# Performance work log

Measured on AMD Instinct MI355X. Metric: run time of the kernel, lower is better.

The kernel has to match this reference:

```python
import jax, jax.numpy as jnp
import numpy as np

L = 2          # MPblock_layers
H = 64         # hidden_channels
B, N, E = 1, 50000, 800000


def setup_inputs() -> dict:
    key = jax.random.key(0)
    ks = jax.random.split(key, 12)
    s = 0.05
    return {
        "x": jax.random.normal(ks[0], (B, N, H), jnp.float32),
        "edge_attr": jax.random.normal(ks[1], (B, E, H), jnp.float32),
        "edge_index": jax.random.randint(ks[2], (2, E), 0, N, jnp.int64 if jax.config.jax_enable_x64 else jnp.int32),
        # per-layer stacked MLP params: edge MLP (3H->H->H), node MLP (2H->H->H)
        "edge_w1": jax.random.normal(ks[3], (L, 3 * H, H), jnp.float32) * s,
        "edge_b1": jnp.zeros((L, H), jnp.float32),
        "edge_w2": jax.random.normal(ks[4], (L, H, H), jnp.float32) * s,
        "edge_b2": jnp.zeros((L, H), jnp.float32),
        "node_w1": jax.random.normal(ks[5], (L, 2 * H, H), jnp.float32) * s,
        "node_b1": jnp.zeros((L, H), jnp.float32),
        "node_w2": jax.random.normal(ks[6], (L, H, H), jnp.float32) * s,
        "node_b2": jnp.zeros((L, H), jnp.float32),
    }


def reference(x, edge_attr, edge_index,
              edge_w1, edge_b1, edge_w2, edge_b2,
              node_w1, node_b1, node_w2, node_b2):
    src = edge_index[0]
    dest = edge_index[1]
    n_nodes = x.shape[1]
    for l in range(L):
        # EdgeModel: cat([edge_attr, x[src], x[dest]]) -> MLP
        cat_e = jnp.concatenate([edge_attr, x[:, src], x[:, dest]], axis=2)  # [B,E,3H]
        h = jax.nn.silu(jnp.einsum('bef,fh->beh', cat_e, edge_w1[l]) + edge_b1[l])
        edge_attr = jnp.einsum('beh,hk->bek', h, edge_w2[l]) + edge_b2[l]      # [B,E,H]
        # NodeModel: scatter_add over dest, cat with x, MLP
        agg = jnp.zeros((x.shape[0], n_nodes, edge_attr.shape[2]), x.dtype).at[:, dest].add(edge_attr)
        cat_n = jnp.concatenate([x, agg], axis=2)                              # [B,N,2H]
        h = jax.nn.silu(jnp.einsum('bnf,fh->bnh', cat_n, node_w1[l]) + node_b1[l])
        x = jnp.einsum('bnh,hk->bnk', h, node_w2[l]) + node_b2[l]              # [B,N,H]
    return (x, edge_attr)
```

## Files before the change

kernel.cpp:

```cpp
#include <hip/hip_runtime.h>

typedef __attribute__((ext_vector_type(8))) _Float16 f16x8;
typedef __attribute__((ext_vector_type(4))) _Float16 f16x4;
typedef __attribute__((ext_vector_type(4))) float f32x4;

#define PWS 72

__device__ __forceinline__ float silu_f(float v) {
    return v * (1.0f / (1.0f + __expf(-v)));
}

__device__ __forceinline__ int xcd_swz(int bid, int nwg) {
    if (nwg < 16) return bid;
    int q = nwg >> 3, r = nwg & 7;
    int x = bid & 7, i = bid >> 3;
    int basex = (x < r) ? x * (q + 1) : r * (q + 1) + (x - r) * q;
    return basex + i;
}

struct WDesc { const float* W; _Float16* out; int K; };
struct WPack { WDesc d[8]; };

__global__ __launch_bounds__(256) void conv_weights(WPack p) {
    WDesc wd = p.d[blockIdx.y];
    int total = wd.K * 64;
    int i = blockIdx.x * 256 + threadIdx.x;
    if (i >= total) return;
    int j  = i & 7;
    int l  = (i >> 3) & 63;
    int tn = i >> 9;
    int t  = tn >> 2, nf = tn & 3;
    int k  = t * 32 + (l >> 4) * 8 + j;
    int c  = nf * 16 + (l & 15);
    wd.out[i] = (_Float16)wd.W[k * 64 + c];
}

__global__ __launch_bounds__(256) void hist_kernel(const int* __restrict__ dst,
                                                   int* __restrict__ counts, int E) {
    int e = blockIdx.x * 256 + threadIdx.x;
    if (e < E) atomicAdd(&counts[dst[e]], 1);
}

__global__ __launch_bounds__(1024) void scan_kernel(int* __restrict__ counts,
                                                    int* __restrict__ row_ptr,
                                                    int N, int E) {
    __shared__ int part[1024];
    int t = threadIdx.x;
    int per = (N + 1023) >> 10;
    int s = t * per, en = min(s + per, N);
    int sum = 0;
    for (int i = s; i < en; ++i) sum += counts[i];
    part[t] = sum;
    __syncthreads();
    for (int off = 1; off < 1024; off <<= 1) {
        int v = (t >= off) ? part[t - off] : 0;
        __syncthreads();
        part[t] += v;
        __syncthreads();
    }
    int run = (t == 0) ? 0 : part[t - 1];
    for (int i = s; i < en; ++i) {
        int c = counts[i];
        row_ptr[i] = run;
        counts[i] = run;
        run += c;
    }
    if (t == 1023) row_ptr[N] = E;
}

__global__ __launch_bounds__(256) void scatter_kernel(
    const int* __restrict__ src, const int* __restrict__ dst,
    int* __restrict__ cursor, int4* __restrict__ pk, int E) {
    int e = blockIdx.x * 256 + threadIdx.x;
    if (e < E) {
        int d = dst[e];
        int pos = atomicAdd(&cursor[d], 1);
        pk[pos] = make_int4(e, src[e], d, 0);
    }
}

template <bool IN16, bool FINAL>
__global__ __launch_bounds__(256, 8) void gnn_edge_sorted(
    const float* __restrict__ x,
    const float* __restrict__ ea0,
    _Float16* __restrict__ ea_mid,
    float* __restrict__ ea_out,
    const int4* __restrict__ pk,
    const _Float16* __restrict__ w1f,
    const float* __restrict__ b1,
    const _Float16* __restrict__ w2f,
    const float* __restrict__ b2,
    int E, int nwg)
{
    __shared__ __align__(16) _Float16 sA[64][PWS];

    const int t    = threadIdx.x;
    const int lane = t & 63;
    const int w    = t >> 6;
    const int col  = lane & 15;
    const int g    = lane >> 4;
    const int ko   = g * 8;
    const int bid  = xcd_swz(blockIdx.x, nwg);
    const long base = (long)bid * 64;

    long p0 = base + w * 16 + col;
    if (p0 >= E) p0 = E - 1;
    int ei0 = 0;
    if constexpr (FINAL) ei0 = pk[p0].x;

    f16x4  ea16v[4];
    float4 ea4[4];
    float4 sx4[4], dx4[4];
#pragma unroll
    for (int it = 0; it < 4; ++it) {
        long p = base + w * 16 + it * 4 + g;
        if (p >= E) p = E - 1;
        int4 rec = pk[p];
        if constexpr (IN16) {
            ea16v[it] = *(const f16x4*)(ea_mid + p * 64 + col * 4);
        } else {
            ea4[it] = *(const float4*)(ea0 + (long)rec.x * 64 + col * 4);
        }
        sx4[it] = *(const float4*)(x + (long)rec.y * 64 + col * 4);
        dx4[it] = *(const float4*)(x + (long)rec.z * 64 + col * 4);
    }

    f32x4 acc[4];
#pragma unroll
    for (int nf = 0; nf < 4; ++nf) {
        float bv = b1[nf * 16 + col];
        acc[nf] = (f32x4){bv, bv, bv, bv};
    }

    const int arow = w * 16 + col;

#define MFMA_L1(s3)                                                             \
    _Pragma("unroll")                                                           \
    for (int tt = 0; tt < 2; ++tt) {                                            \
        int k0 = tt * 32 + ko;                                                  \
        f16x8 af = *(const f16x8*)&sA[arow][k0];                                \
        int tg = (s3) * 2 + tt;                                                 \
        _Pragma("unroll")                                                       \
        for (int nf = 0; nf < 4; ++nf) {                                        \
            f16x8 bf = *(const f16x8*)(w1f + (size_t)((tg*4+nf)*64+lane)*8);    \
            acc[nf] = __builtin_amdgcn_mfma_f32_16x16x32_f16(af, bf, acc[nf], 0, 0, 0); \
        }                                                                       \
    }

#pragma unroll
    for (int it = 0; it < 4; ++it) {
        int rg = w * 16 + it * 4 + g;
        f16x4 hv;
        if constexpr (IN16) {
            hv = ea16v[it];
        } else {
            hv[0] = (_Float16)ea4[it].x; hv[1] = (_Float16)ea4[it].y;
            hv[2] = (_Float16)ea4[it].z; hv[3] = (_Float16)ea4[it].w;
        }
        *(f16x4*)&sA[rg][col * 4] = hv;
    }
    MFMA_L1(0)

#pragma unroll
    for (int it = 0; it < 4; ++it) {
        int rg = w * 16 + it * 4 + g;
        f16x4 hv;
        hv[0] = (_Float16)sx4[it].x; hv[1] = (_Float16)sx4[it].y;
        hv[2] = (_Float16)sx4[it].z; hv[3] = (_Float16)sx4[it].w;
        *(f16x4*)&sA[rg][col * 4] = hv;
    }
    MFMA_L1(1)

#pragma unroll
    for (int it = 0; it < 4; ++it) {
        int rg = w * 16 + it * 4 + g;
        f16x4 hv;
        hv[0] = (_Float16)dx4[it].x; hv[1] = (_Float16)dx4[it].y;
        hv[2] = (_Float16)dx4[it].z; hv[3] = (_Float16)dx4[it].w;
        *(f16x4*)&sA[rg][col * 4] = hv;
    }
    MFMA_L1(2)
#undef MFMA_L1

#pragma unroll
    for (int nf = 0; nf < 4; ++nf)
#pragma unroll
        for (int rg = 0; rg < 4; ++rg) {
            int row = w * 16 + g * 4 + rg;
            sA[row][nf * 16 + col] = (_Float16)silu_f(acc[nf][rg]);
        }

    f32x4 out[4];
#pragma unroll
    for (int nf = 0; nf < 4; ++nf) {
        float bv = b2[nf * 16 + col];
        out[nf] = (f32x4){bv, bv, bv, bv};
    }
#pragma unroll
    for (int tt = 0; tt < 2; ++tt) {
        int k0 = tt * 32 + ko;
        f16x8 af = *(const f16x8*)&sA[arow][k0];
#pragma unroll
        for (int nf = 0; nf < 4; ++nf) {
            f16x8 bf = *(const f16x8*)(w2f + (size_t)((tt * 4 + nf) * 64 + lane) * 8);
            out[nf] = __builtin_amdgcn_mfma_f32_16x16x32_f16(af, bf, out[nf], 0, 0, 0);
        }
    }

    const int rbase = w * 16 + g * 4;
#pragma unroll
    for (int rg = 0; rg < 4; ++rg) {
        long p = base + rbase + rg;
        if (p < E) {
#pragma unroll
            for (int nf = 0; nf < 4; ++nf)
                ea_mid[p * 64 + nf * 16 + col] = (_Float16)out[nf][rg];
            if constexpr (FINAL) {
                int eid = __shfl(ei0, g * 4 + rg);
                float* op = ea_out + (long)eid * 64;
#pragma unroll
                for (int nf = 0; nf < 4; ++nf)
                    op[nf * 16 + col] = out[nf][rg];
            }
        }
    }
}

__global__ __launch_bounds__(256, 4) void gnn_node_fused(
    const float* __restrict__ x_in,
    const _Float16* __restrict__ eaH,
    const int* __restrict__ row_ptr,
    float* __restrict__ x_out,
    const _Float16* __restrict__ w1f,
    const float* __restrict__ b1,
    const _Float16* __restrict__ w2f,
    const float* __restrict__ b2, int N, int nwg)
{
    __shared__ __align__(16) _Float16 sA[64][PWS];

    const int t    = threadIdx.x;
    const int lane = t & 63;
    const int w    = t >> 6;
    const int col  = lane & 15;
    const int g    = lane >> 4;
    const int ko   = g * 8;
    const int bid  = xcd_swz(blockIdx.x, nwg);
    const long base = (long)bid * 64;

    long nr = base + w * 16 + col;
    if (nr >= N) nr = N - 1;
    const float* px = x_in + nr * 64 + ko;

    float4 v0 = *(const float4*)(px);
    float4 v1 = *(const float4*)(px + 4);
    float4 v2 = *(const float4*)(px + 32);
    float4 v3 = *(const float4*)(px + 36);

    int pe0 = row_ptr[nr], pe1 = row_ptr[nr + 1];
    float s0[8], s1[8];
#pragma unroll
    for (int j = 0; j < 8; ++j) { s0[j] = 0.f; s1[j] = 0.f; }
    for (int p = pe0; p < pe1; ++p) {
        f16x8 a = *(const f16x8*)(eaH + (long)p * 64 + ko);
        f16x8 b = *(const f16x8*)(eaH + (long)p * 64 + 32 + ko);
#pragma unroll
        for (int j = 0; j < 8; ++j) { s0[j] += (float)a[j]; s1[j] += (float)b[j]; }
    }

    f32x4 acc[4];
#pragma unroll
    for (int nf = 0; nf < 4; ++nf) {
        float bv = b1[nf * 16 + col];
        acc[nf] = (f32x4){bv, bv, bv, bv};
    }

#define QTRV(m, A, B)                                                           \
    {                                                                           \
        f16x8 af;                                                               \
        af[0] = (_Float16)A.x; af[1] = (_Float16)A.y;                           \
        af[2] = (_Float16)A.z; af[3] = (_Float16)A.w;                           \
        af[4] = (_Float16)B.x; af[5] = (_Float16)B.y;                           \
        af[6] = (_Float16)B.z; af[7] = (_Float16)B.w;                           \
        _Pragma("unroll")                                                       \
        for (int nf = 0; nf < 4; ++nf) {                                        \
            f16x8 bf = *(const f16x8*)(w1f + (size_t)(((m)*4+nf)*64+lane)*8);   \
            acc[nf] = __builtin_amdgcn_mfma_f32_16x16x32_f16(af, bf, acc[nf], 0, 0, 0); \
        }                                                                       \
    }
#define QTRS(m, S)                                                              \
    {                                                                           \
        f16x8 af;                                                               \
        _Pragma("unroll")                                                       \
        for (int j = 0; j < 8; ++j) af[j] = (_Float16)S[j];                     \
        _Pragma("unroll")                                                       \
        for (int nf = 0; nf < 4; ++nf) {                                        \
            f16x8 bf = *(const f16x8*)(w1f + (size_t)(((m)*4+nf)*64+lane)*8);   \
            acc[nf] = __builtin_amdgcn_mfma_f32_16x16x32_f16(af, bf, acc[nf], 0, 0, 0); \
        }                                                                       \
    }
    QTRV(0, v0, v1)  QTRV(1, v2, v3)
    QTRS(2, s0)      QTRS(3, s1)
#undef QTRV
#undef QTRS

#pragma unroll
    for (int nf = 0; nf < 4; ++nf)
#pragma unroll
        for (int rg = 0; rg < 4; ++rg) {
            int row = w * 16 + g * 4 + rg;
            sA[row][nf * 16 + col] = (_Float16)silu_f(acc[nf][rg]);
        }

    f32x4 out[4];
#pragma unroll
    for (int nf = 0; nf < 4; ++nf) {
        float bv = b2[nf * 16 + col];
        out[nf] = (f32x4){bv, bv, bv, bv};
    }
    const int arow = w * 16 + col;
#pragma unroll
    for (int tt = 0; tt < 2; ++tt) {
        int k0 = tt * 32 + ko;
        f16x8 af = *(const f16x8*)&sA[arow][k0];
#pragma unroll
        for (int nf = 0; nf < 4; ++nf) {
            f16x8 bf = *(const f16x8*)(w2f + (size_t)((tt * 4 + nf) * 64 + lane) * 8);
            out[nf] = __builtin_amdgcn_mfma_f32_16x16x32_f16(af, bf, out[nf], 0, 0, 0);
        }
    }

    const int rbase = w * 16 + g * 4;
#pragma unroll
    for (int rg = 0; rg < 4; ++rg) {
        long row = base + rbase + rg;
        if (row < N) {
            float* op = x_out + row * 64;
#pragma unroll
            for (int nf = 0; nf < 4; ++nf)
                op[nf * 16 + col] = out[nf][rg];
        }
    }
}

__global__ __launch_bounds__(256, 8) void gnn_edge_mfma(
    const float* __restrict__ x,
    const float* __restrict__ ea_in,
    float* __restrict__ ea_out,
    const int* __restrict__ src_idx,
    const int* __restrict__ dst_idx,
    const _Float16* __restrict__ w1f,
    const float* __restrict__ b1,
    const _Float16* __restrict__ w2f,
    const float* __restrict__ b2,
    float* __restrict__ agg,
    int E)
{
    __shared__ __align__(16) _Float16 sA[64][PWS];

    const int t    = threadIdx.x;
    const int lane = t & 63;
    const int w    = t >> 6;
    const int col  = lane & 15;
    const int g    = lane >> 4;
    const int ko   = g * 8;
    const long base = (long)blockIdx.x * 64;

    long er0 = base + w * 16 + col;
    if (er0 >= E) er0 = E - 1;
    const int di = dst_idx[er0];

    float4 ea4[4], sx4[4], dx4[4];
#pragma unroll
    for (int it = 0; it < 4; ++it) {
        long er = base + w * 16 + it * 4 + g;
        if (er >= E) er = E - 1;
        ea4[it] = *(const float4*)(ea_in + er * 64 + col * 4);
        sx4[it] = *(const float4*)(x + (long)src_idx[er] * 64 + col * 4);
        dx4[it] = *(const float4*)(x + (long)dst_idx[er] * 64 + col * 4);
    }

    f32x4 acc[4];
#pragma unroll
    for (int nf = 0; nf < 4; ++nf) {
        float bv = b1[nf * 16 + col];
        acc[nf] = (f32x4){bv, bv, bv, bv};
    }
    const int arow = w * 16 + col;

#define MFMA_L1(s3)                                                             \
    _Pragma("unroll")                                                           \
    for (int tt = 0; tt < 2; ++tt) {                                            \
        int k0 = tt * 32 + ko;                                                  \
        f16x8 af = *(const f16x8*)&sA[arow][k0];                                \
        int tg = (s3) * 2 + tt;                                                 \
        _Pragma("unroll")                                                       \
        for (int nf = 0; nf < 4; ++nf) {                                        \
            f16x8 bf = *(const f16x8*)(w1f + (size_t)((tg*4+nf)*64+lane)*8);    \
            acc[nf] = __builtin_amdgcn_mfma_f32_16x16x32_f16(af, bf, acc[nf], 0, 0, 0); \
        }                                                                       \
    }

#pragma unroll
    for (int it = 0; it < 4; ++it) {
        int rg = w * 16 + it * 4 + g;
        f16x4 hv;
        hv[0] = (_Float16)ea4[it].x; hv[1] = (_Float16)ea4[it].y;
        hv[2] = (_Float16)ea4[it].z; hv[3] = (_Float16)ea4[it].w;
        *(f16x4*)&sA[rg][col * 4] = hv;
    }
    MFMA_L1(0)
#pragma unroll
    for (int it = 0; it < 4; ++it) {
        int rg = w * 16 + it * 4 + g;
        f16x4 hv;
        hv[0] = (_Float16)sx4[it].x; hv[1] = (_Float16)sx4[it].y;
        hv[2] = (_Float16)sx4[it].z; hv[3] = (_Float16)sx4[it].w;
        *(f16x4*)&sA[rg][col * 4] = hv;
    }
    MFMA_L1(1)
#pragma unroll
    for (int it = 0; it < 4; ++it) {
        int rg = w * 16 + it * 4 + g;
        f16x4 hv;
        hv[0] = (_Float16)dx4[it].x; hv[1] = (_Float16)dx4[it].y;
        hv[2] = (_Float16)dx4[it].z; hv[3] = (_Float16)dx4[it].w;
        *(f16x4*)&sA[rg][col * 4] = hv;
    }
    MFMA_L1(2)
#undef MFMA_L1

#pragma unroll
    for (int nf = 0; nf < 4; ++nf)
#pragma unroll
        for (int rg = 0; rg < 4; ++rg) {
            int row = w * 16 + g * 4 + rg;
            sA[row][nf * 16 + col] = (_Float16)silu_f(acc[nf][rg]);
        }

    f32x4 out[4];
#pragma unroll
    for (int nf = 0; nf < 4; ++nf) {
        float bv = b2[nf * 16 + col];
        out[nf] = (f32x4){bv, bv, bv, bv};
    }
#pragma unroll
    for (int tt = 0; tt < 2; ++tt) {
        int k0 = tt * 32 + ko;
        f16x8 af = *(const f16x8*)&sA[arow][k0];
#pragma unroll
        for (int nf = 0; nf < 4; ++nf) {
            f16x8 bf = *(const f16x8*)(w2f + (size_t)((tt * 4 + nf) * 64 + lane) * 8);
            out[nf] = __builtin_amdgcn_mfma_f32_16x16x32_f16(af, bf, out[nf], 0, 0, 0);
        }
    }

    const int rbase = w * 16 + g * 4;
#pragma unroll
    for (int rg = 0; rg < 4; ++rg) {
        long row = base + rbase + rg;
        if (row < E) {
            int drow = __shfl(di, g * 4 + rg);
            float* ap = agg + (long)drow * 64;
#pragma unroll
            for (int nf = 0; nf < 4; ++nf) {
                ea_out[row * 64 + nf * 16 + col] = out[nf][rg];
                atomicAdd(&ap[nf * 16 + col], out[nf][rg]);
            }
        }
    }
}

__global__ __launch_bounds__(256, 8) void gnn_node_mfma(
    const float* __restrict__ x_in,
    const float* __restrict__ aggp,
    float* __restrict__ x_out,
    const _Float16* __restrict__ w1f,
    const float* __restrict__ b1,
    const _Float16* __restrict__ w2f,
    const float* __restrict__ b2, int N)
{
    __shared__ __align__(16) _Float16 sA[64][PWS];

    const int t    = threadIdx.x;
    const int lane = t & 63;
    const int w    = t >> 6;
    const int col  = lane & 15;
    const int g    = lane >> 4;
    const int ko   = g * 8;
    const long base = (long)blockIdx.x * 64;

    long nr = base + w * 16 + col;
    if (nr >= N) nr = N - 1;
    const float* px = x_in + nr * 64 + ko;
    const float* pa = aggp + nr * 64 + ko;

    float4 v0 = *(const float4*)(px);
    float4 v1 = *(const float4*)(px + 4);
    float4 v2 = *(const float4*)(px + 32);
    float4 v3 = *(const float4*)(px + 36);
    float4 v4 = *(const float4*)(pa);
    float4 v5 = *(const float4*)(pa + 4);
    float4 v6 = *(const float4*)(pa + 32);
    float4 v7 = *(const float4*)(pa + 36);

    f32x4 acc[4];
#pragma unroll
    for (int nf = 0; nf < 4; ++nf) {
        float bv = b1[nf * 16 + col];
        acc[nf] = (f32x4){bv, bv, bv, bv};
    }

#define QTR(m, A, B)                                                            \
    {                                                                           \
        f16x8 af;                                                               \
        af[0] = (_Float16)A.x; af[1] = (_Float16)A.y;                           \
        af[2] = (_Float16)A.z; af[3] = (_Float16)A.w;                           \
        af[4] = (_Float16)B.x; af[5] = (_Float16)B.y;                           \
        af[6] = (_Float16)B.z; af[7] = (_Float16)B.w;                           \
        _Pragma("unroll")                                                       \
        for (int nf = 0; nf < 4; ++nf) {                                        \
            f16x8 bf = *(const f16x8*)(w1f + (size_t)(((m)*4+nf)*64+lane)*8);   \
            acc[nf] = __builtin_amdgcn_mfma_f32_16x16x32_f16(af, bf, acc[nf], 0, 0, 0); \
        }                                                                       \
    }
    QTR(0, v0, v1)  QTR(1, v2, v3)
    QTR(2, v4, v5)  QTR(3, v6, v7)
#undef QTR

#pragma unroll
    for (int nf = 0; nf < 4; ++nf)
#pragma unroll
        for (int rg = 0; rg < 4; ++rg) {
            int row = w * 16 + g * 4 + rg;
            sA[row][nf * 16 + col] = (_Float16)silu_f(acc[nf][rg]);
        }

    f32x4 out[4];
#pragma unroll
    for (int nf = 0; nf < 4; ++nf) {
        float bv = b2[nf * 16 + col];
        out[nf] = (f32x4){bv, bv, bv, bv};
    }
    const int arow = w * 16 + col;
#pragma unroll
    for (int tt = 0; tt < 2; ++tt) {
        int k0 = tt * 32 + ko;
        f16x8 af = *(const f16x8*)&sA[arow][k0];
#pragma unroll
        for (int nf = 0; nf < 4; ++nf) {
            f16x8 bf = *(const f16x8*)(w2f + (size_t)((tt * 4 + nf) * 64 + lane) * 8);
            out[nf] = __builtin_amdgcn_mfma_f32_16x16x32_f16(af, bf, out[nf], 0, 0, 0);
        }
    }

    const int rbase = w * 16 + g * 4;
#pragma unroll
    for (int rg = 0; rg < 4; ++rg) {
        long row = base + rbase + rg;
        if (row < N) {
            float* op = x_out + row * 64;
#pragma unroll
            for (int nf = 0; nf < 4; ++nf)
                op[nf * 16 + col] = out[nf][rg];
        }
    }
}

extern "C" void kernel_launch(void* const* d_in, const int* in_sizes, int n_in,
                              void* d_out, int out_size, void* d_ws, size_t ws_size,
                              hipStream_t stream) {
    const int H = 64;
    const int N = in_sizes[0] / H;
    const int E = in_sizes[1] / H;

    const float* x0  = (const float*)d_in[0];
    const float* ea0 = (const float*)d_in[1];
    const int*   ei  = (const int*)d_in[2];
    const float* ew1 = (const float*)d_in[3];
    const float* eb1 = (const float*)d_in[4];
    const float* ew2 = (const float*)d_in[5];
    const float* eb2 = (const float*)d_in[6];
    const float* nw1 = (const float*)d_in[7];
    const float* nb1 = (const float*)d_in[8];
    const float* nw2 = (const float*)d_in[9];
    const float* nb2 = (const float*)d_in[10];

    float* outX = (float*)d_out;
    float* outE = outX + (size_t)N * H;

    const size_t aggBytes = (size_t)N * H * sizeof(float);
    const size_t wElems   = 2 * ((size_t)(192 + 64 + 128 + 64) * 64);
    const size_t eaHBytes = (size_t)E * H * sizeof(_Float16);

    float* agg      = (float*)d_ws;
    _Float16* wbase = (_Float16*)((char*)d_ws + aggBytes);
    char* eaH_raw   = (char*)(wbase + wElems);
    eaH_raw = (char*)(((uintptr_t)eaH_raw + 15) & ~(uintptr_t)15);
    _Float16* eaH   = (_Float16*)eaH_raw;
    int* counts     = (int*)(((uintptr_t)((char*)eaH + eaHBytes) + 15) & ~(uintptr_t)15);
    int* row_ptr    = counts + N;
    int4* pk        = (int4*)(((uintptr_t)(row_ptr + N + 1) + 15) & ~(uintptr_t)15);

    const bool sortedOK = ((char*)(pk + E)) <= ((char*)d_ws + ws_size);

    const int* srcI = ei;
    const int* dstI = ei + E;

    WPack pack;
    size_t off = 0;
    _Float16* EW1[2]; _Float16* EW2[2]; _Float16* NW1[2]; _Float16* NW2[2];
    for (int l = 0; l < 2; ++l) {
        EW1[l] = wbase + off; off += 192 * 64;
        EW2[l] = wbase + off; off += 64 * 64;
        NW1[l] = wbase + off; off += 128 * 64;
        NW2[l] = wbase + off; off += 64 * 64;
        pack.d[l * 4 + 0] = {ew1 + (size_t)l * 192 * 64, EW1[l], 192};
        pack.d[l * 4 + 1] = {ew2 + (size_t)l * 64 * 64,  EW2[l], 64};
        pack.d[l * 4 + 2] = {nw1 + (size_t)l * 128 * 64, NW1[l], 128};
        pack.d[l * 4 + 3] = {nw2 + (size_t)l * 64 * 64,  NW2[l], 64};
    }
    conv_weights<<<dim3(48, 8), 256, 0, stream>>>(pack);

    const int egrid = (E + 63) / 64;
    const int ngrid = (N + 63) / 64;

    if (sortedOK) {
        (void)hipMemsetAsync(counts, 0, (size_t)N * sizeof(int), stream);
        hist_kernel<<<(E + 255) / 256, 256, 0, stream>>>(dstI, counts, E);
        scan_kernel<<<1, 1024, 0, stream>>>(counts, row_ptr, N, E);
        scatter_kernel<<<(E + 255) / 256, 256, 0, stream>>>(
            srcI, dstI, counts, pk, E);

        gnn_edge_sorted<false, false><<<egrid, 256, 0, stream>>>(
            x0, ea0, eaH, nullptr, pk,
            EW1[0], eb1, EW2[0], eb2, E, egrid);
        gnn_node_fused<<<ngrid, 256, 0, stream>>>(
            x0, eaH, row_ptr, outX, NW1[0], nb1, NW2[0], nb2, N, ngrid);

        gnn_edge_sorted<true, true><<<egrid, 256, 0, stream>>>(
            outX, nullptr, eaH, outE, pk,
            EW1[1], eb1 + H, EW2[1], eb2 + H, E, egrid);
        gnn_node_fused<<<ngrid, 256, 0, stream>>>(
            outX, eaH, row_ptr, outX, NW1[1], nb1 + H, NW2[1], nb2 + H, N, ngrid);
    } else {
        for (int l = 0; l < 2; ++l) {
            const float* xin  = (l == 0) ? x0  : outX;
            const float* eain = (l == 0) ? ea0 : outE;
            (void)hipMemsetAsync(agg, 0, aggBytes, stream);
            gnn_edge_mfma<<<egrid, 256, 0, stream>>>(
                xin, eain, outE, srcI, dstI,
                EW1[l], eb1 + l * H, EW2[l], eb2 + l * H, agg, E);
            gnn_node_mfma<<<ngrid, 256, 0, stream>>>(
                xin, agg, outX,
                NW1[l], nb1 + l * H, NW2[l], nb2 + l * H, N);
        }
    }
}
```

Baseline: 558.5 us.

## Parallelize CSR scan, read layer-1 edges in original order, unroll aggregation

Measured after the change: 472.2 us. 15.4% less time.

```diff
diff --git a/kernel.cpp b/kernel.cpp
--- a/kernel.cpp
+++ b/kernel.cpp
@@ -41,55 +41,78 @@
     if (e < E) atomicAdd(&counts[dst[e]], 1);
 }
 
-__global__ __launch_bounds__(1024) void scan_kernel(int* __restrict__ counts,
-                                                    int* __restrict__ row_ptr,
-                                                    int N, int E) {
-    __shared__ int part[1024];
+__global__ __launch_bounds__(256) void scan_part(const int* __restrict__ counts,
+                                                 int* __restrict__ partial, int N) {
+    __shared__ int sm[256];
     int t = threadIdx.x;
-    int per = (N + 1023) >> 10;
-    int s = t * per, en = min(s + per, N);
-    int sum = 0;
-    for (int i = s; i < en; ++i) sum += counts[i];
-    part[t] = sum;
+    int i = blockIdx.x * 256 + t;
+    sm[t] = (i < N) ? counts[i] : 0;
     __syncthreads();
-    for (int off = 1; off < 1024; off <<= 1) {
-        int v = (t >= off) ? part[t - off] : 0;
+    for (int off = 128; off > 0; off >>= 1) {
+        if (t < off) sm[t] += sm[t + off];
         __syncthreads();
-        part[t] += v;
+    }
+    if (t == 0) partial[blockIdx.x] = sm[0];
+}
+
+__global__ __launch_bounds__(256) void scan_mid(int* __restrict__ partial, int nP) {
+    __shared__ int sm[256];
+    int t = threadIdx.x;
+    int v = (t < nP) ? partial[t] : 0;
+    sm[t] = v;
+    __syncthreads();
+    for (int off = 1; off < 256; off <<= 1) {
+        int add = (t >= off) ? sm[t - off] : 0;
         __syncthreads();
-    }
-    int run = (t == 0) ? 0 : part[t - 1];
-    for (int i = s; i < en; ++i) {
-        int c = counts[i];
-        row_ptr[i] = run;
-        counts[i] = run;
-        run += c;
-    }
-    if (t == 1023) row_ptr[N] = E;
+        sm[t] += add;
+        __syncthreads();
+    }
+    if (t < nP) partial[t] = sm[t] - v;
+}
+
+__global__ __launch_bounds__(256) void scan_fin(int* __restrict__ counts,
+                                                const int* __restrict__ partial,
+                                                int* __restrict__ row_ptr,
+                                                int N, int E) {
+    __shared__ int sm[256];
+    int t = threadIdx.x;
+    int i = blockIdx.x * 256 + t;
+    int v = (i < N) ? counts[i] : 0;
+    sm[t] = v;
+    __syncthreads();
+    for (int off = 1; off < 256; off <<= 1) {
+        int add = (t >= off) ? sm[t - off] : 0;
+        __syncthreads();
+        sm[t] += add;
+        __syncthreads();
+    }
+    int excl = sm[t] - v + partial[blockIdx.x];
+    if (i < N) { row_ptr[i] = excl; counts[i] = excl; }
+    if (blockIdx.x == 0 && t == 0) row_ptr[N] = E;
 }
 
 __global__ __launch_bounds__(256) void scatter_kernel(
     const int* __restrict__ src, const int* __restrict__ dst,
-    int* __restrict__ cursor, int4* __restrict__ pk, int E) {
+    int* __restrict__ cursor, int4* __restrict__ pk,
+    int* __restrict__ posA, int E) {
     int e = blockIdx.x * 256 + threadIdx.x;
     if (e < E) {
         int d = dst[e];
         int pos = atomicAdd(&cursor[d], 1);
         pk[pos] = make_int4(e, src[e], d, 0);
-    }
-}
-
-template <bool IN16, bool FINAL>
-__global__ __launch_bounds__(256, 8) void gnn_edge_sorted(
+        posA[e] = pos;
+    }
+}
+
+__global__ __launch_bounds__(256, 8) void gnn_edge_l1(
     const float* __restrict__ x,
-    const float* __restrict__ ea0,
+    const float* __restrict__ ea_in,
     _Float16* __restrict__ ea_mid,
-    float* __restrict__ ea_out,
-    const int4* __restrict__ pk,
-    const _Float16* __restrict__ w1f,
-    const float* __restrict__ b1,
-    const _Float16* __restrict__ w2f,
-    const float* __restrict__ b2,
+    const int* __restrict__ src_idx,
+    const int* __restrict__ dst_idx,
+    const int* __restrict__ posA,
+    const _Float16* __restrict__ w1f, const float* __restrict__ b1,
+    const _Float16* __restrict__ w2f, const float* __restrict__ b2,
     int E, int nwg)
 {
     __shared__ __align__(16) _Float16 sA[64][PWS];
@@ -103,26 +126,18 @@
     const int bid  = xcd_swz(blockIdx.x, nwg);
     const long base = (long)bid * 64;
 
-    long p0 = base + w * 16 + col;
-    if (p0 >= E) p0 = E - 1;
-    int ei0 = 0;
-    if constexpr (FINAL) ei0 = pk[p0].x;
-
-    f16x4  ea16v[4];
-    float4 ea4[4];
-    float4 sx4[4], dx4[4];
-#pragma unroll
-    for (int it = 0; it < 4; ++it) {
-        long p = base + w * 16 + it * 4 + g;
-        if (p >= E) p = E - 1;
-        int4 rec = pk[p];
-        if constexpr (IN16) {
-            ea16v[it] = *(const f16x4*)(ea_mid + p * 64 + col * 4);
-        } else {
-            ea4[it] = *(const float4*)(ea0 + (long)rec.x * 64 + col * 4);
-        }
-        sx4[it] = *(const float4*)(x + (long)rec.y * 64 + col * 4);
-        dx4[it] = *(const float4*)(x + (long)rec.z * 64 + col * 4);
+    long er0 = base + w * 16 + col;
+    if (er0 >= E) er0 = E - 1;
+    const int p0 = posA[er0];
+
+    float4 ea4[4], sx4[4], dx4[4];
+#pragma unroll
+    for (int it = 0; it < 4; ++it) {
+        long er = base + w * 16 + it * 4 + g;
+        if (er >= E) er = E - 1;
+        ea4[it] = *(const float4*)(ea_in + er * 64 + col * 4);
+        sx4[it] = *(const float4*)(x + (long)src_idx[er] * 64 + col * 4);
+        dx4[it] = *(const float4*)(x + (long)dst_idx[er] * 64 + col * 4);
     }
 
     f32x4 acc[4];
@@ -131,7 +146,6 @@
         float bv = b1[nf * 16 + col];
         acc[nf] = (f32x4){bv, bv, bv, bv};
     }
-
     const int arow = w * 16 + col;
 
 #define MFMA_L1(s3)                                                             \
@@ -151,16 +165,11 @@
     for (int it = 0; it < 4; ++it) {
         int rg = w * 16 + it * 4 + g;
         f16x4 hv;
-        if constexpr (IN16) {
-            hv = ea16v[it];
-        } else {
-            hv[0] = (_Float16)ea4[it].x; hv[1] = (_Float16)ea4[it].y;
-            hv[2] = (_Float16)ea4[it].z; hv[3] = (_Float16)ea4[it].w;
-        }
+        hv[0] = (_Float16)ea4[it].x; hv[1] = (_Float16)ea4[it].y;
+        hv[2] = (_Float16)ea4[it].z; hv[3] = (_Float16)ea4[it].w;
         *(f16x4*)&sA[rg][col * 4] = hv;
     }
     MFMA_L1(0)
-
 #pragma unroll
     for (int it = 0; it < 4; ++it) {
         int rg = w * 16 + it * 4 + g;
@@ -170,7 +179,6 @@
         *(f16x4*)&sA[rg][col * 4] = hv;
     }
     MFMA_L1(1)
-
 #pragma unroll
     for (int it = 0; it < 4; ++it) {
         int rg = w * 16 + it * 4 + g;
@@ -210,31 +218,24 @@
     const int rbase = w * 16 + g * 4;
 #pragma unroll
     for (int rg = 0; rg < 4; ++rg) {
-        long p = base + rbase + rg;
-        if (p < E) {
+        long row = base + rbase + rg;
+        if (row < E) {
+            int pp = __shfl(p0, g * 4 + rg);
 #pragma unroll
             for (int nf = 0; nf < 4; ++nf)
-                ea_mid[p * 64 + nf * 16 + col] = (_Float16)out[nf][rg];
-            if constexpr (FINAL) {
-                int eid = __shfl(ei0, g * 4 + rg);
-                float* op = ea_out + (long)eid * 64;
-#pragma unroll
-                for (int nf = 0; nf < 4; ++nf)
-                    op[nf * 16 + col] = out[nf][rg];
-            }
-        }
-    }
-}
-
-__global__ __launch_bounds__(256, 4) void gnn_node_fused(
-    const float* __restrict__ x_in,
-    const _Float16* __restrict__ eaH,
-    const int* __restrict__ row_ptr,
-    float* __restrict__ x_out,
-    const _Float16* __restrict__ w1f,
-    const float* __restrict__ b1,
-    const _Float16* __restrict__ w2f,
-    const float* __restrict__ b2, int N, int nwg)
+                ea_mid[(long)pp * 64 + nf * 16 + col] = (_Float16)out[nf][rg];
+        }
+    }
+}
+
+__global__ __launch_bounds__(256, 8) void gnn_edge_l2(
+    const float* __restrict__ x,
+    _Float16* __restrict__ ea_mid,
+    float* __restrict__ ea_out,
+    const int4* __restrict__ pk,
+    const _Float16* __restrict__ w1f, const float* __restrict__ b1,
+    const _Float16* __restrict__ w2f, const float* __restrict__ b2,
+    int E, int nwg)
 {
     __shared__ __align__(16) _Float16 sA[64][PWS];
 
@@ -247,6 +248,131 @@
     const int bid  = xcd_swz(blockIdx.x, nwg);
     const long base = (long)bid * 64;
 
+    long p0 = base + w * 16 + col;
+    if (p0 >= E) p0 = E - 1;
+    const int ei0 = pk[p0].x;
+
+    f16x4  ea16v[4];
+    float4 sx4[4], dx4[4];
+#pragma unroll
+    for (int it = 0; it < 4; ++it) {
+        long p = base + w * 16 + it * 4 + g;
+        if (p >= E) p = E - 1;
+        int4 rec = pk[p];
+        ea16v[it] = *(const f16x4*)(ea_mid + p * 64 + col * 4);
+        sx4[it] = *(const float4*)(x + (long)rec.y * 64 + col * 4);
+        dx4[it] = *(const float4*)(x + (long)rec.z * 64 + col * 4);
+    }
+
+    f32x4 acc[4];
+#pragma unroll
+    for (int nf = 0; nf < 4; ++nf) {
+        float bv = b1[nf * 16 + col];
+        acc[nf] = (f32x4){bv, bv, bv, bv};
+    }
+    const int arow = w * 16 + col;
+
+#define MFMA_L1(s3)                                                             \
+    _Pragma("unroll")                                                           \
+    for (int tt = 0; tt < 2; ++tt) {                                            \
+        int k0 = tt * 32 + ko;                                                  \
+        f16x8 af = *(const f16x8*)&sA[arow][k0];                                \
+        int tg = (s3) * 2 + tt;                                                 \
+        _Pragma("unroll")                                                       \
+        for (int nf = 0; nf < 4; ++nf) {                                        \
+            f16x8 bf = *(const f16x8*)(w1f + (size_t)((tg*4+nf)*64+lane)*8);    \
+            acc[nf] = __builtin_amdgcn_mfma_f32_16x16x32_f16(af, bf, acc[nf], 0, 0, 0); \
+        }                                                                       \
+    }
+
+#pragma unroll
+    for (int it = 0; it < 4; ++it) {
+        int rg = w * 16 + it * 4 + g;
+        *(f16x4*)&sA[rg][col * 4] = ea16v[it];
+    }
+    MFMA_L1(0)
+#pragma unroll
+    for (int it = 0; it < 4; ++it) {
+        int rg = w * 16 + it * 4 + g;
+        f16x4 hv;
+        hv[0] = (_Float16)sx4[it].x; hv[1] = (_Float16)sx4[it].y;
+        hv[2] = (_Float16)sx4[it].z; hv[3] = (_Float16)sx4[it].w;
+        *(f16x4*)&sA[rg][col * 4] = hv;
+    }
+    MFMA_L1(1)
+#pragma unroll
+    for (int it = 0; it < 4; ++it) {
+        int rg = w * 16 + it * 4 + g;
+        f16x4 hv;
+        hv[0] = (_Float16)dx4[it].x; hv[1] = (_Float16)dx4[it].y;
+        hv[2] = (_Float16)dx4[it].z; hv[3] = (_Float16)dx4[it].w;
+        *(f16x4*)&sA[rg][col * 4] = hv;
+    }
+    MFMA_L1(2)
+#undef MFMA_L1
+
+#pragma unroll
+    for (int nf = 0; nf < 4; ++nf)
+#pragma unroll
+        for (int rg = 0; rg < 4; ++rg) {
+            int row = w * 16 + g * 4 + rg;
+            sA[row][nf * 16 + col] = (_Float16)silu_f(acc[nf][rg]);
+        }
+
+    f32x4 out[4];
+#pragma unroll
+    for (int nf = 0; nf < 4; ++nf) {
+        float bv = b2[nf * 16 + col];
+        out[nf] = (f32x4){bv, bv, bv, bv};
+    }
+#pragma unroll
+    for (int tt = 0; tt < 2; ++tt) {
+        int k0 = tt * 32 + ko;
+        f16x8 af = *(const f16x8*)&sA[arow][k0];
+#pragma unroll
+        for (int nf = 0; nf < 4; ++nf) {
+            f16x8 bf = *(const f16x8*)(w2f + (size_t)((tt * 4 + nf) * 64 + lane) * 8);
+            out[nf] = __builtin_amdgcn_mfma_f32_16x16x32_f16(af, bf, out[nf], 0, 0, 0);
+        }
+    }
+
+    const int rbase = w * 16 + g * 4;
+#pragma unroll
+    for (int rg = 0; rg < 4; ++rg) {
+        long p = base + rbase + rg;
+        if (p < E) {
+#pragma unroll
+            for (int nf = 0; nf < 4; ++nf)
+                ea_mid[p * 64 + nf * 16 + col] = (_Float16)out[nf][rg];
+            int eid = __shfl(ei0, g * 4 + rg);
+            float* op = ea_out + (long)eid * 64;
+#pragma unroll
+            for (int nf = 0; nf < 4; ++nf)
+                op[nf * 16 + col] = out[nf][rg];
+        }
+    }
+}
+
+__global__ __launch_bounds__(256, 4) void gnn_node_fused(
+    const float* __restrict__ x_in,
+    const _Float16* __restrict__ eaH,
+    const int* __restrict__ row_ptr,
+    float* __restrict__ x_out,
+    const _Float16* __restrict__ w1f, const float* __restrict__ b1,
+    const _Float16* __restrict__ w2f, const float* __restrict__ b2,
+    int N, int nwg)
+{
+    __shared__ __align__(16) _Float16 sA[64][PWS];
+
+    const int t    = threadIdx.x;
+    const int lane = t & 63;
+    const int w    = t >> 6;
+    const int col  = lane & 15;
+    const int g    = lane >> 4;
+    const int ko   = g * 8;
+    const int bid  = xcd_swz(blockIdx.x, nwg);
+    const long base = (long)bid * 64;
+
     long nr = base + w * 16 + col;
     if (nr >= N) nr = N - 1;
     const float* px = x_in + nr * 64 + ko;
@@ -260,11 +386,23 @@
     float s0[8], s1[8];
 #pragma unroll
     for (int j = 0; j < 8; ++j) { s0[j] = 0.f; s1[j] = 0.f; }
-    for (int p = pe0; p < pe1; ++p) {
-        f16x8 a = *(const f16x8*)(eaH + (long)p * 64 + ko);
-        f16x8 b = *(const f16x8*)(eaH + (long)p * 64 + 32 + ko);
-#pragma unroll
-        for (int j = 0; j < 8; ++j) { s0[j] += (float)a[j]; s1[j] += (float)b[j]; }
+    int p = pe0;
+    for (; p + 2 <= pe1; p += 2) {
+        f16x8 a0 = *(const f16x8*)(eaH + (long)p * 64 + ko);
+        f16x8 b0 = *(const f16x8*)(eaH + (long)p * 64 + 32 + ko);
+        f16x8 a1 = *(const f16x8*)(eaH + (long)(p + 1) * 64 + ko);
+        f16x8 b1v = *(const f16x8*)(eaH + (long)(p + 1) * 64 + 32 + ko);
+#pragma unroll
+        for (int j = 0; j < 8; ++j) {
+            s0[j] += (float)a0[j] + (float)a1[j];
+            s1[j] += (float)b0[j] + (float)b1v[j];
+        }
+    }
+    if (p < pe1) {
+        f16x8 a0 = *(const f16x8*)(eaH + (long)p * 64 + ko);
+        f16x8 b0 = *(const f16x8*)(eaH + (long)p * 64 + 32 + ko);
+#pragma unroll
+        for (int j = 0; j < 8; ++j) { s0[j] += (float)a0[j]; s1[j] += (float)b0[j]; }
     }
 
     f32x4 acc[4];
@@ -348,12 +486,9 @@
     float* __restrict__ ea_out,
     const int* __restrict__ src_idx,
     const int* __restrict__ dst_idx,
-    const _Float16* __restrict__ w1f,
-    const float* __restrict__ b1,
-    const _Float16* __restrict__ w2f,
-    const float* __restrict__ b2,
-    float* __restrict__ agg,
-    int E)
+    const _Float16* __restrict__ w1f, const float* __restrict__ b1,
+    const _Float16* __restrict__ w2f, const float* __restrict__ b2,
+    float* __restrict__ agg, int E)
 {
     __shared__ __align__(16) _Float16 sA[64][PWS];
 
@@ -474,10 +609,8 @@
     const float* __restrict__ x_in,
     const float* __restrict__ aggp,
     float* __restrict__ x_out,
-    const _Float16* __restrict__ w1f,
-    const float* __restrict__ b1,
-    const _Float16* __restrict__ w2f,
-    const float* __restrict__ b2, int N)
+    const _Float16* __restrict__ w1f, const float* __restrict__ b1,
+    const _Float16* __restrict__ w2f, const float* __restrict__ b2, int N)
 {
     __shared__ __align__(16) _Float16 sA[64][PWS];
 
@@ -599,7 +732,9 @@
     _Float16* eaH   = (_Float16*)eaH_raw;
     int* counts     = (int*)(((uintptr_t)((char*)eaH + eaHBytes) + 15) & ~(uintptr_t)15);
     int* row_ptr    = counts + N;
-    int4* pk        = (int4*)(((uintptr_t)(row_ptr + N + 1) + 15) & ~(uintptr_t)15);
+    int* partial    = row_ptr + N + 1;
+    int* posA       = partial + 256;
+    int4* pk        = (int4*)(((uintptr_t)(posA + E) + 15) & ~(uintptr_t)15);
 
     const bool sortedOK = ((char*)(pk + E)) <= ((char*)d_ws + ws_size);
 
@@ -623,22 +758,25 @@
 
     const int egrid = (E + 63) / 64;
     const int ngrid = (N + 63) / 64;
+    const int sgrid = (N + 255) / 256;
 
     if (sortedOK) {
         (void)hipMemsetAsync(counts, 0, (size_t)N * sizeof(int), stream);
         hist_kernel<<<(E + 255) / 256, 256, 0, stream>>>(dstI, counts, E);
-        scan_kernel<<<1, 1024, 0, stream>>>(counts, row_ptr, N, E);
+        scan_part<<<sgrid, 256, 0, stream>>>(counts, partial, N);
+        scan_mid<<<1, 256, 0, stream>>>(partial, sgrid);
+        scan_fin<<<sgrid, 256, 0, stream>>>(counts, partial, row_ptr, N, E);
         scatter_kernel<<<(E + 255) / 256, 256, 0, stream>>>(
-            srcI, dstI, counts, pk, E);
-
-        gnn_edge_sorted<false, false><<<egrid, 256, 0, stream>>>(
-            x0, ea0, eaH, nullptr, pk,
+            srcI, dstI, counts, pk, posA, E);
+
+        gnn_edge_l1<<<egrid, 256, 0, stream>>>(
+            x0, ea0, eaH, srcI, dstI, posA,
             EW1[0], eb1, EW2[0], eb2, E, egrid);
         gnn_node_fused<<<ngrid, 256, 0, stream>>>(
             x0, eaH, row_ptr, outX, NW1[0], nb1, NW2[0], nb2, N, ngrid);
 
-        gnn_edge_sorted<true, true><<<egrid, 256, 0, stream>>>(
-            outX, nullptr, eaH, outE, pk,
+        gnn_edge_l2<<<egrid, 256, 0, stream>>>(
+            outX, eaH, outE, pk,
             EW1[1], eb1 + H, EW2[1], eb2 + H, E, egrid);
         gnn_node_fused<<<ngrid, 256, 0, stream>>>(
             outX, eaH, row_ptr, outX, NW1[1], nb1 + H, NW2[1], nb2 + H, N, ngrid);
```
